# Performance work log

Measured on AMD Instinct MI355X. Metric: run time of the kernel, lower is better.

## Reference

```python
import jax, jax.numpy as jnp
import numpy as np

MAX_DISTANCE = 10
SCALE = 0.01

def distance_bias(seq_len):
    # |i - j| clamped to MAX_DISTANCE, scaled
    idx = jnp.arange(seq_len, dtype=jnp.float32)
    d = jnp.abs(idx[None, :] - idx[:, None])
    return jnp.clip(d, 0.0, MAX_DISTANCE) * SCALE  # [S, S]

def setup_inputs() -> dict:
    key = jax.random.key(0)
    k1, k2 = jax.random.split(key)
    B, S, D_IN, D_OUT = 8, 2048, 1024, 1024
    x = jax.random.normal(k1, (B, S, D_IN), dtype=jnp.float32)
    W = jax.random.normal(k2, (D_IN, D_OUT), dtype=jnp.float32) * (1.0 / np.sqrt(D_IN))
    b = jnp.zeros((D_OUT,), dtype=jnp.float32)
    return {"x": x, "W": W, "b": b}

def reference(x, W, b):
    B, S, _ = x.shape
    f = x @ W + b                                   # [B, S, H]
    e = jnp.einsum('bsd,btd->bst', f, f)            # scores [B, S, S]
    e = e + distance_bias(S)[None, :, :]
    a = jax.nn.softmax(e, axis=-1)
    out = jnp.einsum('bst,btd->bsd', a, f)          # weighted sum [B, S, H]
    return out
```

## Files before the change

### kernel.cpp

```cpp
#include <hip/hip_runtime.h>
#include <hip/hip_bf16.h>
#include <stdint.h>

typedef __attribute__((ext_vector_type(8))) short bf16x8;
typedef __attribute__((ext_vector_type(4))) float f32x4;

static __device__ __forceinline__ unsigned short f2bf(float f) {
  union { float f; unsigned int u; } v; v.f = f;
  unsigned int u = v.u;
  u += 0x7FFFu + ((u >> 16) & 1u);
  return (unsigned short)(u >> 16);
}
static __device__ __forceinline__ float bf2f(unsigned short h) {
  union { unsigned int u; float f; } v; v.u = ((unsigned int)h) << 16; return v.f;
}

typedef __attribute__((address_space(1))) void gvoid;
typedef __attribute__((address_space(3))) void lvoid;
static __device__ __forceinline__ void gload_lds16(const void* gp, void* lp) {
  __builtin_amdgcn_global_load_lds((gvoid*)gp, (lvoid*)lp, 16, 0, 0);
}

__global__ __launch_bounds__(256) void k_convX(const float* __restrict__ X,
                                               unsigned short* __restrict__ Xb) {
  size_t i = ((size_t)blockIdx.x * 256 + threadIdx.x) * 8;
  const size_t stride = (size_t)4096 * 256 * 8;
  for (; i < (size_t)16777216; i += stride) {
    float4 v0 = *(const float4*)(X + i), v1 = *(const float4*)(X + i + 4);
    unsigned short h[8];
    h[0]=f2bf(v0.x); h[1]=f2bf(v0.y); h[2]=f2bf(v0.z); h[3]=f2bf(v0.w);
    h[4]=f2bf(v1.x); h[5]=f2bf(v1.y); h[6]=f2bf(v1.z); h[7]=f2bf(v1.w);
    *(uint4*)(Xb + i) = *(uint4*)h;
  }
}

__global__ __launch_bounds__(256) void k_convW(const float* __restrict__ W,
                                               unsigned short* __restrict__ Wt) {
  __shared__ __align__(16) unsigned short lds[64][72];
  const int tid = threadIdx.x;
  const int n0 = blockIdx.x * 64, k0 = blockIdx.y * 64;
  for (int i = 0; i < 4; ++i) {
    int c = i * 256 + tid;
    int r = c >> 4, c4 = (c & 15) * 4;
    float4 v = *(const float4*)(W + (size_t)(k0 + r) * 1024 + n0 + c4);
    unsigned short* p = &lds[r][c4];
    p[0] = f2bf(v.x); p[1] = f2bf(v.y); p[2] = f2bf(v.z); p[3] = f2bf(v.w);
  }
  __syncthreads();
  for (int i = 0; i < 2; ++i) {
    int c = i * 256 + tid;
    int n = c >> 3, k8 = (c & 7) * 8;
    unsigned short tmp[8];
    for (int j = 0; j < 8; ++j) tmp[j] = lds[k8 + j][n];
    *(uint4*)(Wt + (size_t)(n0 + n) * 1024 + k0 + k8) = *(uint4*)tmp;
  }
}

__global__ __launch_bounds__(256) void k_transF(const unsigned short* __restrict__ F,
                                                unsigned short* __restrict__ Ft) {
  __shared__ __align__(16) unsigned short lds[64][72];
  const int tid = threadIdx.x;
  const int t0 = blockIdx.x * 64, d0 = blockIdx.y * 64;
  const unsigned short* Fb = F + (size_t)blockIdx.z * 2048 * 1024;
  unsigned short* Ftb = Ft + (size_t)blockIdx.z * 1024 * 2048;
  for (int i = 0; i < 2; ++i) {
    int c = i * 256 + tid;
    int r = c >> 3, d8 = (c & 7) * 8;
    *(uint4*)(&lds[r][d8]) = *(const uint4*)(Fb + (size_t)(t0 + r) * 1024 + d0 + d8);
  }
  __syncthreads();
  for (int i = 0; i < 2; ++i) {
    int c = i * 256 + tid;
    int d = c >> 3, t8 = (c & 7) * 8;
    unsigned short tmp[8];
    for (int j = 0; j < 8; ++j) tmp[j] = lds[t8 + j][d];
    *(uint4*)(Ftb + (size_t)(d0 + d) * 2048 + t0 + t8) = *(uint4*)tmp;
  }
}


template<int NT>
__device__ __forceinline__ void gemm_core(
    const unsigned short* __restrict__ Ag, int lda, int ar0,
    const unsigned short* __restrict__ Bg, int ldb, int br0,
    unsigned short* __restrict__ As, unsigned short* __restrict__ Bs,
    f32x4 (&acc)[8][4]) {
  const int tid = threadIdx.x, lane = tid & 63, wid = tid >> 6;
  const int wr = wid >> 2, wc = wid & 3;
  const int rl = lane & 15;
  const int rslot = (((lane >> 4) ^ (lane & 3) ^ ((lane >> 2) & 3))) * 8;
  const int q = tid >> 2;
  const int sslot = (((tid & 3) ^ (q & 3) ^ ((q >> 2) & 3))) * 8;

#define STAGE_T(dstbase, src, ld, r0, kt)                                      \
  _Pragma("unroll")                                                            \
  for (int r_ = 0; r_ < 2; ++r_)                                               \
    gload_lds16((src) + (size_t)((r0) + r_ * 128 + q) * (ld) + (kt) * 32 + sslot, \
                (char*)(dstbase) + r_ * 8192 + wid * 1024);

  STAGE_T(As + 0 * 8192, Ag, lda, ar0, 0)
  STAGE_T(Bs + 0 * 8192, Bg, ldb, br0, 0)
  STAGE_T(As + 1 * 8192, Ag, lda, ar0, 1)
  STAGE_T(Bs + 1 * 8192, Bg, ldb, br0, 1)
  STAGE_T(As + 2 * 8192, Ag, lda, ar0, 2)
  STAGE_T(Bs + 2 * 8192, Bg, ldb, br0, 2)
  asm volatile("s_waitcnt vmcnt(8)" ::: "memory");
  __builtin_amdgcn_s_barrier();

  bf16x8 a[4], b[4], a2[4];
  for (int t = 0; t < NT; ++t) {
    const int sl = t & 3;
    const int ps = (t + 3 < NT) ? (t + 3) : (NT - 1);
    const int psl = (t + 3) & 3;
    const unsigned short* Ab = As + sl * 8192;
    const unsigned short* Bb = Bs + sl * 8192;
#pragma unroll
    for (int m = 0; m < 4; ++m)
      a[m] = *(const bf16x8*)(Ab + (wr * 128 + m * 16 + rl) * 32 + rslot);
#pragma unroll
    for (int n = 0; n < 4; ++n)
      b[n] = *(const bf16x8*)(Bb + (wc * 64 + n * 16 + rl) * 32 + rslot);
    STAGE_T(As + psl * 8192, Ag, lda, ar0, ps)
    __builtin_amdgcn_s_barrier();
    asm volatile("s_waitcnt lgkmcnt(0)" ::: "memory");
    __builtin_amdgcn_s_setprio(1);
#pragma unroll
    for (int m = 0; m < 4; ++m)
#pragma unroll
      for (int n = 0; n < 4; ++n)
        acc[m][n] = __builtin_amdgcn_mfma_f32_16x16x32_bf16(a[m], b[n], acc[m][n], 0, 0, 0);
    __builtin_amdgcn_s_setprio(0);
    __builtin_amdgcn_s_barrier();
#pragma unroll
    for (int m = 0; m < 4; ++m)
      a2[m] = *(const bf16x8*)(Ab + (wr * 128 + (m + 4) * 16 + rl) * 32 + rslot);
    STAGE_T(Bs + psl * 8192, Bg, ldb, br0, ps)
    __builtin_amdgcn_s_barrier();
    asm volatile("s_waitcnt lgkmcnt(0)" ::: "memory");
    __builtin_amdgcn_s_setprio(1);
#pragma unroll
    for (int m = 0; m < 4; ++m)
#pragma unroll
      for (int n = 0; n < 4; ++n)
        acc[m + 4][n] = __builtin_amdgcn_mfma_f32_16x16x32_bf16(a2[m], b[n], acc[m + 4][n], 0, 0, 0);
    __builtin_amdgcn_s_setprio(0);
    asm volatile("s_waitcnt vmcnt(8)" ::: "memory");
    __builtin_amdgcn_s_barrier();
  }
  asm volatile("s_waitcnt vmcnt(0)" ::: "memory");
#undef STAGE_T
}

__global__ __launch_bounds__(512, 2) void k_gemm1(const unsigned short* __restrict__ Xb,
                                                  const unsigned short* __restrict__ Wt,
                                                  const float* __restrict__ bias,
                                                  unsigned short* __restrict__ F) {
  __shared__ __align__(16) unsigned short As[4 * 8192];
  __shared__ __align__(16) unsigned short Bs[4 * 8192];
  const int bid = blockIdx.x;
  const int swz = (bid & 7) * 32 + (bid >> 3);
  const int m0 = (swz >> 2) * 256, n0 = (swz & 3) * 256;
  f32x4 acc[8][4] = {};
  gemm_core<32>(Xb, 1024, m0, Wt, 1024, n0, As, Bs, acc);
  const int tid = threadIdx.x, lane = tid & 63, wid = tid >> 6;
  const int wr = wid >> 2, wc = wid & 3;
  const int r4 = (lane >> 4) * 4, cl = lane & 15;
#pragma unroll
  for (int n = 0; n < 4; ++n) {
    int col = n0 + wc * 64 + n * 16 + cl;
    float bv = bias[col];
#pragma unroll
    for (int m = 0; m < 8; ++m) {
      int row = m0 + wr * 128 + m * 16 + r4;
#pragma unroll
      for (int j = 0; j < 4; ++j)
        F[(size_t)(row + j) * 1024 + col] = f2bf(acc[m][n][j] + bv);
    }
  }
}

__global__ __launch_bounds__(512, 2) void k_gemm2(const unsigned short* __restrict__ F,
                                                  unsigned short* __restrict__ E) {
  __shared__ __align__(16) unsigned short As[4 * 8192];
  __shared__ __align__(16) unsigned short Bs[4 * 8192];
  const int bid = blockIdx.x;
  const int z = bid & 7;
  int rem = bid >> 3, bi = 0;
  while (rem >= 8 - bi) { rem -= 8 - bi; ++bi; }
  const int bj = bi + rem;
  const int m0 = bi * 256, n0 = bj * 256;
  const unsigned short* Fb = F + (size_t)z * 2048 * 1024;
  unsigned short* Eb = E + (size_t)z * 2048 * 2048;
  f32x4 acc[8][4] = {};
  gemm_core<32>(Fb, 1024, m0, Fb, 1024, n0, As, Bs, acc);
  const int tid = threadIdx.x, lane = tid & 63, wid = tid >> 6;
  const int wr = wid >> 2, wc = wid & 3;
  const int r4 = (lane >> 4) * 4, cl = lane & 15;
#pragma unroll
  for (int m = 0; m < 8; ++m) {
    int row = m0 + wr * 128 + m * 16 + r4;
#pragma unroll
    for (int n = 0; n < 4; ++n) {
      int col = n0 + wc * 64 + n * 16 + cl;
#pragma unroll
      for (int j = 0; j < 4; ++j) {
        int rr = row + j;
        int d = rr - col; d = d < 0 ? -d : d; d = d > 10 ? 10 : d;
        Eb[(size_t)rr * 2048 + col] = f2bf(acc[m][n][j] + (float)d * 0.01f);
      }
    }
  }
  if (bi == bj) return;
  __syncthreads();
  unsigned short* lt = As;
  for (int c = 0; c < 4; ++c) {
    if (wr == (c >> 1)) {
      const int mbase = (c & 1) * 4;
#pragma unroll
      for (int mm = 0; mm < 4; ++mm) {
        const int m = mbase + mm;
        const int row = m0 + wr * 128 + m * 16 + r4;
#pragma unroll
        for (int n = 0; n < 4; ++n) {
          const int col = wc * 64 + n * 16 + cl;
          const int colg = n0 + col;
          unsigned short hh[4];
#pragma unroll
          for (int j = 0; j < 4; ++j) {
            int rr = row + j;
            int d = rr - colg; d = d < 0 ? -d : d; d = d > 10 ? 10 : d;
            hh[j] = f2bf(acc[m][n][j] + (float)d * 0.01f);
          }
          *(uint2*)(lt + col * 72 + mm * 16 + r4) = *(uint2*)hh;
        }
      }
    }
    __syncthreads();
    const int oc = tid >> 1, h = tid & 1;
    unsigned short* dst = Eb + (size_t)(n0 + oc) * 2048 + m0 + c * 64 + h * 32;
    const unsigned short* srcL = lt + oc * 72 + h * 32;
#pragma unroll
    for (int i = 0; i < 4; ++i)
      *(uint4*)(dst + i * 8) = *(const uint4*)(srcL + i * 8);
    __syncthreads();
  }
}

__global__ __launch_bounds__(256) void k_softmax(unsigned short* __restrict__ E) {
  const int tid = threadIdx.x, lane = tid & 63, w = tid >> 6;
  unsigned short* row = E + ((size_t)blockIdx.x * 4 + w) * 2048;
  uint4 v[4];
  float f[32];
#pragma unroll
  for (int i = 0; i < 4; ++i) {
    v[i] = ((const uint4*)row)[i * 64 + lane];
    const unsigned int* up = (const unsigned int*)&v[i];
#pragma unroll
    for (int k = 0; k < 4; ++k) {
      f[i * 8 + 2 * k]     = bf2f((unsigned short)(up[k] & 0xFFFF));
      f[i * 8 + 2 * k + 1] = bf2f((unsigned short)(up[k] >> 16));
    }
  }
  float mx = f[0];
#pragma unroll
  for (int i = 1; i < 32; ++i) mx = fmaxf(mx, f[i]);
  for (int s = 32; s > 0; s >>= 1) mx = fmaxf(mx, __shfl_xor(mx, s));
  float sum = 0.f;
#pragma unroll
  for (int i = 0; i < 32; ++i) { f[i] = __expf(f[i] - mx); sum += f[i]; }
  for (int s = 32; s > 0; s >>= 1) sum += __shfl_xor(sum, s);
  const float inv = 1.0f / sum;
#pragma unroll
  for (int i = 0; i < 4; ++i) {
    unsigned short hh[8];
#pragma unroll
    for (int k = 0; k < 8; ++k) hh[k] = f2bf(f[i * 8 + k] * inv);
    ((uint4*)row)[i * 64 + lane] = *(uint4*)hh;
  }
}

__global__ __launch_bounds__(512, 2) void k_gemm3(const unsigned short* __restrict__ P,
                                                  const unsigned short* __restrict__ Ft,
                                                  float* __restrict__ out) {
  __shared__ __align__(16) unsigned short As[4 * 8192];
  __shared__ __align__(16) unsigned short Bs[4 * 8192];
  const int bid = blockIdx.x;
  const int swz = (bid & 7) * 32 + (bid >> 3);
  const int z = swz >> 5;
  const int m0 = ((swz >> 2) & 7) * 256, n0 = (swz & 3) * 256;
  const unsigned short* Pb = P + (size_t)z * 2048 * 2048;
  const unsigned short* Ftb = Ft + (size_t)z * 1024 * 2048;
  float* outb = out + (size_t)z * 2048 * 1024;
  f32x4 acc[8][4] = {};
  gemm_core<64>(Pb, 2048, m0, Ftb, 2048, n0, As, Bs, acc);
  const int tid = threadIdx.x, lane = tid & 63, wid = tid >> 6;
  const int wr = wid >> 2, wc = wid & 3;
  const int r4 = (lane >> 4) * 4, cl = lane & 15;
#pragma unroll
  for (int m = 0; m < 8; ++m) {
    int row = m0 + wr * 128 + m * 16 + r4;
#pragma unroll
    for (int n = 0; n < 4; ++n) {
      int col = n0 + wc * 64 + n * 16 + cl;
#pragma unroll
      for (int j = 0; j < 4; ++j)
        outb[(size_t)(row + j) * 1024 + col] = acc[m][n][j];
    }
  }
}

extern "C" void kernel_launch(void* const* d_in, const int* in_sizes, int n_in,
                              void* d_out, int out_size, void* d_ws, size_t ws_size,
                              hipStream_t stream) {
  const float* x = (const float*)d_in[0];
  const float* W = (const float*)d_in[1];
  const float* b = (const float*)d_in[2];
  float* out = (float*)d_out;

  unsigned short* Wt = (unsigned short*)d_ws;
  unsigned short* F  = (unsigned short*)((char*)d_ws + (2ull   << 20));
  unsigned short* Ft = (unsigned short*)((char*)d_ws + (34ull  << 20));
  unsigned short* E  = (unsigned short*)((char*)d_ws + (66ull  << 20));
  unsigned short* Xb = (unsigned short*)((char*)d_ws + (130ull << 20));

  k_convW  <<<dim3(16, 16),    256, 0, stream>>>(W, Wt);
  k_convX  <<<dim3(4096),      256, 0, stream>>>(x, Xb);
  k_gemm1  <<<dim3(256),       512, 0, stream>>>(Xb, Wt, b, F);
  k_transF <<<dim3(32, 16, 8), 256, 0, stream>>>(F, Ft);
  k_gemm2  <<<dim3(288),       512, 0, stream>>>(F, E);
  k_softmax<<<dim3(4096),      256, 0, stream>>>(E);
  k_gemm3  <<<dim3(256),       512, 0, stream>>>(E, Ft, out);
}
```

Before: 436.6 us.

## Compute score GEMM in FP8 e4m3 over full grid instead of symmetric bf16

The first GEMM now also writes an FP8 e4m3 copy of F, and the score GEMM reads that copy and runs fp8 MFMA with its own staging loop. It also drops the symmetric upper-triangle trick: all 512 tiles are computed directly, with no LDS transpose for mirrored tiles. The aim is to halve operand bytes and use the faster fp8 MFMA rate. The cost is more tiles, an extra byte-wide F8 write in gemm1, and much coarser scores, which may hurt softmax accuracy (e4m3 flushes values below 2^-6 and clamps at 448).

```diff
diff --git a/kernel.cpp b/kernel.cpp
--- a/kernel.cpp
+++ b/kernel.cpp
@@ -13,6 +13,18 @@
 }
 static __device__ __forceinline__ float bf2f(unsigned short h) {
   union { unsigned int u; float f; } v; v.u = ((unsigned int)h) << 16; return v.f;
+}
+static __device__ __forceinline__ unsigned char f2e4m3(float f) {
+  union { float f; unsigned int u; } v; v.f = f;
+  unsigned int s = (v.u >> 24) & 0x80u;
+  float a = fabsf(f);
+  if (!(a >= 0.015625f)) return (unsigned char)s;
+  if (a > 448.f) a = 448.f;
+  v.f = a;
+  unsigned int m = v.u + (0x000FFFFFu + ((v.u >> 20) & 1u));
+  m >>= 20;
+  int e = (int)(m >> 3) - 127 + 7;
+  return (unsigned char)(s | ((unsigned)e << 4) | (m & 7u));
 }
 
 typedef __attribute__((address_space(1))) void gvoid;
@@ -77,7 +89,6 @@
     *(uint4*)(Ftb + (size_t)(d0 + d) * 2048 + t0 + t8) = *(uint4*)tmp;
   }
 }
-
 
 template<int NT>
 __device__ __forceinline__ void gemm_core(
@@ -154,7 +165,8 @@
 __global__ __launch_bounds__(512, 2) void k_gemm1(const unsigned short* __restrict__ Xb,
                                                   const unsigned short* __restrict__ Wt,
                                                   const float* __restrict__ bias,
-                                                  unsigned short* __restrict__ F) {
+                                                  unsigned short* __restrict__ F,
+                                                  unsigned char* __restrict__ F8) {
   __shared__ __align__(16) unsigned short As[4 * 8192];
   __shared__ __align__(16) unsigned short Bs[4 * 8192];
   const int bid = blockIdx.x;
@@ -173,28 +185,87 @@
     for (int m = 0; m < 8; ++m) {
       int row = m0 + wr * 128 + m * 16 + r4;
 #pragma unroll
-      for (int j = 0; j < 4; ++j)
-        F[(size_t)(row + j) * 1024 + col] = f2bf(acc[m][n][j] + bv);
+      for (int j = 0; j < 4; ++j) {
+        float val = acc[m][n][j] + bv;
+        F [(size_t)(row + j) * 1024 + col] = f2bf(val);
+        F8[(size_t)(row + j) * 1024 + col] = f2e4m3(val);
+      }
     }
   }
 }
 
-__global__ __launch_bounds__(512, 2) void k_gemm2(const unsigned short* __restrict__ F,
-                                                  unsigned short* __restrict__ E) {
-  __shared__ __align__(16) unsigned short As[4 * 8192];
-  __shared__ __align__(16) unsigned short Bs[4 * 8192];
+__global__ __launch_bounds__(512) void k_gemm2(const unsigned char* __restrict__ F8,
+                                               unsigned short* __restrict__ E) {
+  __shared__ __align__(16) unsigned char As8[4 * 8192];
+  __shared__ __align__(16) unsigned char Bs8[4 * 8192];
   const int bid = blockIdx.x;
-  const int z = bid & 7;
-  int rem = bid >> 3, bi = 0;
-  while (rem >= 8 - bi) { rem -= 8 - bi; ++bi; }
-  const int bj = bi + rem;
-  const int m0 = bi * 256, n0 = bj * 256;
-  const unsigned short* Fb = F + (size_t)z * 2048 * 1024;
+  const int swz = (bid & 7) * 64 + (bid >> 3);
+  const int z = swz >> 6;
+  const int m0 = ((swz >> 3) & 7) * 256, n0 = (swz & 7) * 256;
+  const unsigned char* Fb = F8 + (size_t)z * 2048 * 1024;
   unsigned short* Eb = E + (size_t)z * 2048 * 2048;
-  f32x4 acc[8][4] = {};
-  gemm_core<32>(Fb, 1024, m0, Fb, 1024, n0, As, Bs, acc);
   const int tid = threadIdx.x, lane = tid & 63, wid = tid >> 6;
   const int wr = wid >> 2, wc = wid & 3;
+  const int rl = lane & 15;
+  const int slot8 = (lane >> 4) * 8;
+  f32x4 acc[8][4] = {};
+
+#define STAGE8(dstbase, r0, kt)                                                \
+  gload_lds16(Fb + (size_t)((r0) + (tid >> 1)) * 1024 + (kt) * 32 + (tid & 1) * 16, \
+              (char*)(dstbase) + tid * 16);
+
+  STAGE8(As8 + 0 * 8192, m0, 0)
+  STAGE8(Bs8 + 0 * 8192, n0, 0)
+  STAGE8(As8 + 1 * 8192, m0, 1)
+  STAGE8(Bs8 + 1 * 8192, n0, 1)
+  STAGE8(As8 + 2 * 8192, m0, 2)
+  STAGE8(Bs8 + 2 * 8192, n0, 2)
+  asm volatile("s_waitcnt vmcnt(4)" ::: "memory");
+  __builtin_amdgcn_s_barrier();
+
+  long long a[4], b[4], a2[4];
+  for (int t = 0; t < 32; ++t) {
+    const int sl = t & 3;
+    const int ps = (t + 3 < 32) ? (t + 3) : 31;
+    const int psl = (t + 3) & 3;
+    const unsigned char* Ab = As8 + sl * 8192;
+    const unsigned char* Bb = Bs8 + sl * 8192;
+#pragma unroll
+    for (int m = 0; m < 4; ++m)
+      a[m] = *(const long long*)(Ab + (wr * 128 + m * 16 + rl) * 32 + slot8);
+#pragma unroll
+    for (int n = 0; n < 4; ++n)
+      b[n] = *(const long long*)(Bb + (wc * 64 + n * 16 + rl) * 32 + slot8);
+    STAGE8(As8 + psl * 8192, m0, ps)
+    __builtin_amdgcn_s_barrier();
+    asm volatile("s_waitcnt lgkmcnt(0)" ::: "memory");
+    __builtin_amdgcn_s_setprio(1);
+#pragma unroll
+    for (int m = 0; m < 4; ++m)
+#pragma unroll
+      for (int n = 0; n < 4; ++n)
+        acc[m][n] = __builtin_amdgcn_mfma_f32_16x16x32_fp8_fp8(a[m], b[n], acc[m][n], 0, 0, 0);
+    __builtin_amdgcn_s_setprio(0);
+    __builtin_amdgcn_s_barrier();
+#pragma unroll
+    for (int m = 0; m < 4; ++m)
+      a2[m] = *(const long long*)(Ab + (wr * 128 + (m + 4) * 16 + rl) * 32 + slot8);
+    STAGE8(Bs8 + psl * 8192, n0, ps)
+    __builtin_amdgcn_s_barrier();
+    asm volatile("s_waitcnt lgkmcnt(0)" ::: "memory");
+    __builtin_amdgcn_s_setprio(1);
+#pragma unroll
+    for (int m = 0; m < 4; ++m)
+#pragma unroll
+      for (int n = 0; n < 4; ++n)
+        acc[m + 4][n] = __builtin_amdgcn_mfma_f32_16x16x32_fp8_fp8(a2[m], b[n], acc[m + 4][n], 0, 0, 0);
+    __builtin_amdgcn_s_setprio(0);
+    asm volatile("s_waitcnt vmcnt(4)" ::: "memory");
+    __builtin_amdgcn_s_barrier();
+  }
+  asm volatile("s_waitcnt vmcnt(0)" ::: "memory");
+#undef STAGE8
+
   const int r4 = (lane >> 4) * 4, cl = lane & 15;
 #pragma unroll
   for (int m = 0; m < 8; ++m) {
@@ -209,40 +280,6 @@
         Eb[(size_t)rr * 2048 + col] = f2bf(acc[m][n][j] + (float)d * 0.01f);
       }
     }
-  }
-  if (bi == bj) return;
-  __syncthreads();
-  unsigned short* lt = As;
-  for (int c = 0; c < 4; ++c) {
-    if (wr == (c >> 1)) {
-      const int mbase = (c & 1) * 4;
-#pragma unroll
-      for (int mm = 0; mm < 4; ++mm) {
-        const int m = mbase + mm;
-        const int row = m0 + wr * 128 + m * 16 + r4;
-#pragma unroll
-        for (int n = 0; n < 4; ++n) {
-          const int col = wc * 64 + n * 16 + cl;
-          const int colg = n0 + col;
-          unsigned short hh[4];
-#pragma unroll
-          for (int j = 0; j < 4; ++j) {
-            int rr = row + j;
-            int d = rr - colg; d = d < 0 ? -d : d; d = d > 10 ? 10 : d;
-            hh[j] = f2bf(acc[m][n][j] + (float)d * 0.01f);
-          }
-          *(uint2*)(lt + col * 72 + mm * 16 + r4) = *(uint2*)hh;
-        }
-      }
-    }
-    __syncthreads();
-    const int oc = tid >> 1, h = tid & 1;
-    unsigned short* dst = Eb + (size_t)(n0 + oc) * 2048 + m0 + c * 64 + h * 32;
-    const unsigned short* srcL = lt + oc * 72 + h * 32;
-#pragma unroll
-    for (int i = 0; i < 4; ++i)
-      *(uint4*)(dst + i * 8) = *(const uint4*)(srcL + i * 8);
-    __syncthreads();
   }
 }
 
@@ -322,12 +359,13 @@
   unsigned short* Ft = (unsigned short*)((char*)d_ws + (34ull  << 20));
   unsigned short* E  = (unsigned short*)((char*)d_ws + (66ull  << 20));
   unsigned short* Xb = (unsigned short*)((char*)d_ws + (130ull << 20));
+  unsigned char*  F8 = (unsigned char*) ((char*)d_ws + (162ull << 20));
 
   k_convW  <<<dim3(16, 16),    256, 0, stream>>>(W, Wt);
   k_convX  <<<dim3(4096),      256, 0, stream>>>(x, Xb);
-  k_gemm1  <<<dim3(256),       512, 0, stream>>>(Xb, Wt, b, F);
+  k_gemm1  <<<dim3(256),       512, 0, stream>>>(Xb, Wt, b, F, F8);
   k_transF <<<dim3(32, 16, 8), 256, 0, stream>>>(F, Ft);
-  k_gemm2  <<<dim3(288),       512, 0, stream>>>(F, E);
+  k_gemm2  <<<dim3(512),       512, 0, stream>>>(F8, E);
   k_softmax<<<dim3(4096),      256, 0, stream>>>(E);
   k_gemm3  <<<dim3(256),       512, 0, stream>>>(E, Ft, out);
 }
```

Measured after the change: 366.6 us. 1.19x faster.

## Fuse F transpose into gemm1 epilogue and retile gemm2 as full grid

Applied to the files above, without the earlier changes.

The separate transpose kernel is removed; gemm1's epilogue now also writes the transposed F (Ft) directly with 8-byte stores. gemm2 no longer exploits the symmetry of F·Fᵀ. It computes every 256x128 tile with a smaller double-buffered LDS pipeline, which allows higher occupancy, and drops the mirrored transposed-tile writes. This removes one launch and one full pass over F but roughly doubles the MFMA work in gemm2. The Ft writes from gemm1 are strided, column-wise scattered stores.

```diff
diff --git a/kernel.cpp b/kernel.cpp
--- a/kernel.cpp
+++ b/kernel.cpp
@@ -55,29 +55,6 @@
     *(uint4*)(Wt + (size_t)(n0 + n) * 1024 + k0 + k8) = *(uint4*)tmp;
   }
 }
-
-__global__ __launch_bounds__(256) void k_transF(const unsigned short* __restrict__ F,
-                                                unsigned short* __restrict__ Ft) {
-  __shared__ __align__(16) unsigned short lds[64][72];
-  const int tid = threadIdx.x;
-  const int t0 = blockIdx.x * 64, d0 = blockIdx.y * 64;
-  const unsigned short* Fb = F + (size_t)blockIdx.z * 2048 * 1024;
-  unsigned short* Ftb = Ft + (size_t)blockIdx.z * 1024 * 2048;
-  for (int i = 0; i < 2; ++i) {
-    int c = i * 256 + tid;
-    int r = c >> 3, d8 = (c & 7) * 8;
-    *(uint4*)(&lds[r][d8]) = *(const uint4*)(Fb + (size_t)(t0 + r) * 1024 + d0 + d8);
-  }
-  __syncthreads();
-  for (int i = 0; i < 2; ++i) {
-    int c = i * 256 + tid;
-    int d = c >> 3, t8 = (c & 7) * 8;
-    unsigned short tmp[8];
-    for (int j = 0; j < 8; ++j) tmp[j] = lds[t8 + j][d];
-    *(uint4*)(Ftb + (size_t)(d0 + d) * 2048 + t0 + t8) = *(uint4*)tmp;
-  }
-}
-
 
 template<int NT>
 __device__ __forceinline__ void gemm_core(
@@ -154,7 +131,8 @@
 __global__ __launch_bounds__(512, 2) void k_gemm1(const unsigned short* __restrict__ Xb,
                                                   const unsigned short* __restrict__ Wt,
                                                   const float* __restrict__ bias,
-                                                  unsigned short* __restrict__ F) {
+                                                  unsigned short* __restrict__ F,
+                                                  unsigned short* __restrict__ Ft) {
   __shared__ __align__(16) unsigned short As[4 * 8192];
   __shared__ __align__(16) unsigned short Bs[4 * 8192];
   const int bid = blockIdx.x;
@@ -172,36 +150,80 @@
 #pragma unroll
     for (int m = 0; m < 8; ++m) {
       int row = m0 + wr * 128 + m * 16 + r4;
-#pragma unroll
-      for (int j = 0; j < 4; ++j)
-        F[(size_t)(row + j) * 1024 + col] = f2bf(acc[m][n][j] + bv);
+      __align__(8) unsigned short hh[4];
+#pragma unroll
+      for (int j = 0; j < 4; ++j) hh[j] = f2bf(acc[m][n][j] + bv);
+#pragma unroll
+      for (int j = 0; j < 4; ++j) F[(size_t)(row + j) * 1024 + col] = hh[j];
+      const int z = row >> 11, s = row & 2047;
+      *(uint2*)(Ft + ((size_t)z * 1024 + col) * 2048 + s) = *(const uint2*)hh;
     }
   }
 }
 
-__global__ __launch_bounds__(512, 2) void k_gemm2(const unsigned short* __restrict__ F,
+__global__ __launch_bounds__(512, 6) void k_gemm2(const unsigned short* __restrict__ F,
                                                   unsigned short* __restrict__ E) {
-  __shared__ __align__(16) unsigned short As[4 * 8192];
-  __shared__ __align__(16) unsigned short Bs[4 * 8192];
+  __shared__ __align__(16) unsigned short As2[2][8192];
+  __shared__ __align__(16) unsigned short Bs2[2][4096];
   const int bid = blockIdx.x;
-  const int z = bid & 7;
-  int rem = bid >> 3, bi = 0;
-  while (rem >= 8 - bi) { rem -= 8 - bi; ++bi; }
-  const int bj = bi + rem;
-  const int m0 = bi * 256, n0 = bj * 256;
+  const int swz = (bid & 7) * 128 + (bid >> 3);
+  const int z = swz >> 7;
+  const int m0 = ((swz >> 4) & 7) * 256, n0 = (swz & 15) * 128;
   const unsigned short* Fb = F + (size_t)z * 2048 * 1024;
   unsigned short* Eb = E + (size_t)z * 2048 * 2048;
-  f32x4 acc[8][4] = {};
-  gemm_core<32>(Fb, 1024, m0, Fb, 1024, n0, As, Bs, acc);
   const int tid = threadIdx.x, lane = tid & 63, wid = tid >> 6;
   const int wr = wid >> 2, wc = wid & 3;
+  const int rl = lane & 15;
+  const int rslot = ((lane >> 4) ^ (lane & 3) ^ ((lane >> 2) & 3)) * 8;
+  const int q = tid >> 2;
+  const int sslot = ((tid & 3) ^ (q & 3) ^ ((q >> 2) & 3)) * 8;
+  f32x4 acc[8][2] = {};
+
+#define STAGE_A2(buf, kt)                                                      \
+  _Pragma("unroll")                                                            \
+  for (int r_ = 0; r_ < 2; ++r_)                                               \
+    gload_lds16(Fb + (size_t)(m0 + r_ * 128 + q) * 1024 + (kt) * 32 + sslot,   \
+                (char*)(As2[buf]) + r_ * 8192 + wid * 1024);
+#define STAGE_B2(buf, kt)                                                      \
+  gload_lds16(Fb + (size_t)(n0 + q) * 1024 + (kt) * 32 + sslot,                \
+              (char*)(Bs2[buf]) + wid * 1024);
+
+  STAGE_A2(0, 0)
+  STAGE_B2(0, 0)
+  asm volatile("s_waitcnt vmcnt(0)" ::: "memory");
+  __builtin_amdgcn_s_barrier();
+
+  for (int t = 0; t < 32; ++t) {
+    const int cur = t & 1;
+    bf16x8 a[8], b[2];
+#pragma unroll
+    for (int m = 0; m < 8; ++m)
+      a[m] = *(const bf16x8*)(&As2[cur][(wr * 128 + m * 16 + rl) * 32 + rslot]);
+#pragma unroll
+    for (int n = 0; n < 2; ++n)
+      b[n] = *(const bf16x8*)(&Bs2[cur][(wc * 32 + n * 16 + rl) * 32 + rslot]);
+    if (t < 31) { STAGE_A2(cur ^ 1, t + 1) STAGE_B2(cur ^ 1, t + 1) }
+    asm volatile("s_waitcnt lgkmcnt(0)" ::: "memory");
+    __builtin_amdgcn_s_setprio(1);
+#pragma unroll
+    for (int m = 0; m < 8; ++m)
+#pragma unroll
+      for (int n = 0; n < 2; ++n)
+        acc[m][n] = __builtin_amdgcn_mfma_f32_16x16x32_bf16(a[m], b[n], acc[m][n], 0, 0, 0);
+    __builtin_amdgcn_s_setprio(0);
+    if (t < 31) asm volatile("s_waitcnt vmcnt(0)" ::: "memory");
+    __builtin_amdgcn_s_barrier();
+  }
+#undef STAGE_A2
+#undef STAGE_B2
+
   const int r4 = (lane >> 4) * 4, cl = lane & 15;
 #pragma unroll
   for (int m = 0; m < 8; ++m) {
     int row = m0 + wr * 128 + m * 16 + r4;
 #pragma unroll
-    for (int n = 0; n < 4; ++n) {
-      int col = n0 + wc * 64 + n * 16 + cl;
+    for (int n = 0; n < 2; ++n) {
+      int col = n0 + wc * 32 + n * 16 + cl;
 #pragma unroll
       for (int j = 0; j < 4; ++j) {
         int rr = row + j;
@@ -209,40 +231,6 @@
         Eb[(size_t)rr * 2048 + col] = f2bf(acc[m][n][j] + (float)d * 0.01f);
       }
     }
-  }
-  if (bi == bj) return;
-  __syncthreads();
-  unsigned short* lt = As;
-  for (int c = 0; c < 4; ++c) {
-    if (wr == (c >> 1)) {
-      const int mbase = (c & 1) * 4;
-#pragma unroll
-      for (int mm = 0; mm < 4; ++mm) {
-        const int m = mbase + mm;
-        const int row = m0 + wr * 128 + m * 16 + r4;
-#pragma unroll
-        for (int n = 0; n < 4; ++n) {
-          const int col = wc * 64 + n * 16 + cl;
-          const int colg = n0 + col;
-          unsigned short hh[4];
-#pragma unroll
-          for (int j = 0; j < 4; ++j) {
-            int rr = row + j;
-            int d = rr - colg; d = d < 0 ? -d : d; d = d > 10 ? 10 : d;
-            hh[j] = f2bf(acc[m][n][j] + (float)d * 0.01f);
-          }
-          *(uint2*)(lt + col * 72 + mm * 16 + r4) = *(uint2*)hh;
-        }
-      }
-    }
-    __syncthreads();
-    const int oc = tid >> 1, h = tid & 1;
-    unsigned short* dst = Eb + (size_t)(n0 + oc) * 2048 + m0 + c * 64 + h * 32;
-    const unsigned short* srcL = lt + oc * 72 + h * 32;
-#pragma unroll
-    for (int i = 0; i < 4; ++i)
-      *(uint4*)(dst + i * 8) = *(const uint4*)(srcL + i * 8);
-    __syncthreads();
   }
 }
 
@@ -323,11 +311,10 @@
   unsigned short* E  = (unsigned short*)((char*)d_ws + (66ull  << 20));
   unsigned short* Xb = (unsigned short*)((char*)d_ws + (130ull << 20));
 
-  k_convW  <<<dim3(16, 16),    256, 0, stream>>>(W, Wt);
-  k_convX  <<<dim3(4096),      256, 0, stream>>>(x, Xb);
-  k_gemm1  <<<dim3(256),       512, 0, stream>>>(Xb, Wt, b, F);
-  k_transF <<<dim3(32, 16, 8), 256, 0, stream>>>(F, Ft);
-  k_gemm2  <<<dim3(288),       512, 0, stream>>>(F, E);
-  k_softmax<<<dim3(4096),      256, 0, stream>>>(E);
-  k_gemm3  <<<dim3(256),       512, 0, stream>>>(E, Ft, out);
-}
+  k_convW  <<<dim3(16, 16), 256, 0, stream>>>(W, Wt);
+  k_convX  <<<dim3(4096),   256, 0, stream>>>(x, Xb);
+  k_gemm1  <<<dim3(256),    512, 0, stream>>>(Xb, Wt, b, F, Ft);
+  k_gemm2  <<<dim3(1024),   512, 0, stream>>>(F, E);
+  k_softmax<<<dim3(4096),   256, 0, stream>>>(E);
+  k_gemm3  <<<dim3(256),    512, 0, stream>>>(E, Ft, out);
+}
```

Result: slower. 997.2 us (+128.4%).
